# Optimization experiments

Hardware: AMD Instinct MI355X
Metric: run time of the kernel (lower is better)

Reference implementation:

```python
import jax, jax.numpy as jnp
import numpy as np

D_MODEL = 1024
HEAD = 16
EPS = 1e-6


def _norm(x, alpha, beta):
    # Faithful to NormalizeLayer: torch.std is unbiased (ddof=1); scalar alpha/bias.
    mean = jnp.mean(x, axis=-1, keepdims=True)
    std = jnp.std(x, axis=-1, ddof=1, keepdims=True)
    return alpha * ((x - mean) / (std + EPS)) + beta


def setup_inputs() -> dict:
    key = jax.random.key(0)
    ks = jax.random.split(key, 16)
    B, S, D = 4, 1024, D_MODEL
    s = 1.0 / np.sqrt(D)
    inp = {
        'x': jax.random.normal(ks[0], (B, S, D), dtype=jnp.float32),
        'mask': jnp.ones((B, 1, 1, S), dtype=jnp.int32),
        'Wq_w': jax.random.normal(ks[1], (D, D), dtype=jnp.float32) * s,
        'Wq_b': jnp.zeros((D,), dtype=jnp.float32),
        'Wk_w': jax.random.normal(ks[2], (D, D), dtype=jnp.float32) * s,
        'Wk_b': jnp.zeros((D,), dtype=jnp.float32),
        'Wv_w': jax.random.normal(ks[3], (D, D), dtype=jnp.float32) * s,
        'Wv_b': jnp.zeros((D,), dtype=jnp.float32),
        'Wo_w': jax.random.normal(ks[4], (D, D), dtype=jnp.float32) * s,
        'Wo_b': jnp.zeros((D,), dtype=jnp.float32),
        'ff1_w': jax.random.normal(ks[5], (D, D), dtype=jnp.float32) * s,
        'ff1_b': jnp.zeros((D,), dtype=jnp.float32),
        'ff2_w': jax.random.normal(ks[6], (D, D), dtype=jnp.float32) * s,
        'ff2_b': jnp.zeros((D,), dtype=jnp.float32),
        'alpha1': jnp.ones((1,), dtype=jnp.float32),
        'beta1': jnp.zeros((1,), dtype=jnp.float32),
        'alpha2': jnp.ones((1,), dtype=jnp.float32),
        'beta2': jnp.zeros((1,), dtype=jnp.float32),
    }
    return inp


def reference(x, mask, Wq_w, Wq_b, Wk_w, Wk_b, Wv_w, Wv_b, Wo_w, Wo_b,
              ff1_w, ff1_b, ff2_w, ff2_b, alpha1, beta1, alpha2, beta2):
    B, S, D = x.shape
    H = HEAD
    kd = D // H
    # QKV projections (torch Linear: y = x @ W.T + b)
    Q = (x @ Wq_w.T + Wq_b).reshape(B, S, H, kd).transpose(0, 2, 1, 3)
    K = (x @ Wk_w.T + Wk_b).reshape(B, S, H, kd).transpose(0, 2, 1, 3)
    V = (x @ Wv_w.T + Wv_b).reshape(B, S, H, kd).transpose(0, 2, 1, 3)
    score = jnp.einsum('bhqd,bhkd->bhqk', Q, K) / jnp.sqrt(jnp.float32(kd))
    score = jnp.where(mask == 0, -jnp.inf, score)
    attn = jax.nn.softmax(score, axis=-1)
    o = jnp.einsum('bhqk,bhkd->bhqd', attn, V)
    o = o.transpose(0, 2, 1, 3).reshape(B, S, D)
    attn_out = o @ Wo_w.T + Wo_b
    # residual 1 + custom norm (dropout is identity in eval / drop=0)
    x1 = _norm(x + attn_out, alpha1, beta1)
    # feed-forward: Linear -> ReLU -> Linear (both d_model x d_model)
    ff = jax.nn.relu(x1 @ ff1_w.T + ff1_b) @ ff2_w.T + ff2_b
    # residual 2 + custom norm
    return _norm(x1 + ff, alpha2, beta2)
```

## Files before the change

### kernel.cpp

```cpp
#include <hip/hip_runtime.h>


typedef __bf16 bf16x8 __attribute__((ext_vector_type(8)));
typedef float f32x4 __attribute__((ext_vector_type(4)));
typedef unsigned short ushort4v __attribute__((ext_vector_type(4)));

static __device__ __forceinline__ unsigned short f2bf(float f) {
  return __builtin_bit_cast(unsigned short, (__bf16)f);
}
static __device__ __forceinline__ float bf2f(unsigned short u) {
  return __builtin_bit_cast(float, (unsigned int)u << 16);
}

static __device__ __forceinline__ void gload_lds16(const void* g, void* l) {
  __builtin_amdgcn_global_load_lds(
      (const __attribute__((address_space(1))) unsigned int*)g,
      (__attribute__((address_space(3))) unsigned int*)l, 16, 0, 0);
}

__global__ __launch_bounds__(256)
void cvt_all(const float* __restrict__ x, const float* __restrict__ wq,
             const float* __restrict__ wk, const float* __restrict__ wv,
             const float* __restrict__ wo, const float* __restrict__ w1,
             const float* __restrict__ w2,
             unsigned short* __restrict__ x_bf, unsigned short* __restrict__ wqkv_bf,
             unsigned short* __restrict__ wo_bf, unsigned short* __restrict__ w1_bf,
             unsigned short* __restrict__ w2_bf) {
  const int y = blockIdx.y;
  const size_t MEL = 1u << 20;
  const float* src;
  unsigned short* dst;
  switch (y) {
    case 0: case 1: case 2: case 3: src = x + y * MEL; dst = x_bf + y * MEL; break;
    case 4: src = wq; dst = wqkv_bf; break;
    case 5: src = wk; dst = wqkv_bf + MEL; break;
    case 6: src = wv; dst = wqkv_bf + 2 * MEL; break;
    case 7: src = wo; dst = wo_bf; break;
    case 8: src = w1; dst = w1_bf; break;
    default: src = w2; dst = w2_bf; break;
  }
  const int i = blockIdx.x * 256 + threadIdx.x;
  const float4 v = reinterpret_cast<const float4*>(src)[i];
  ushort4v o;
  o[0] = f2bf(v.x); o[1] = f2bf(v.y); o[2] = f2bf(v.z); o[3] = f2bf(v.w);
  reinterpret_cast<ushort4v*>(dst)[i] = o;
}

template<bool RELU, int OUT_MODE>
__global__ __launch_bounds__(256, 2)
void gemm_bt(const unsigned short* __restrict__ A,
             const unsigned short* __restrict__ W,
             const float* __restrict__ bias0, const float* __restrict__ bias1,
             const float* __restrict__ bias2,
             void* __restrict__ out0, unsigned short* __restrict__ outK,
             unsigned short* __restrict__ outVt, int M, int N, int K) {
  __shared__ __align__(16) unsigned short Al[2][128][64];
  __shared__ __align__(16) unsigned short Bl[2][128][64];
  const int tid = threadIdx.x;
  const int lane = tid & 63;
  const int w = tid >> 6;
  const int wr = w >> 1, wc = w & 1;
  const int grp = lane >> 4, l15 = lane & 15;
  const long bRow = (long)blockIdx.x * 128;
  const long bCol = (long)blockIdx.y * 128;

  f32x4 acc[4][4];
#pragma unroll
  for (int m = 0; m < 4; m++)
#pragma unroll
    for (int n = 0; n < 4; n++) { f32x4 z = {0.f,0.f,0.f,0.f}; acc[m][n] = z; }

  const int srow = tid >> 3;
  const int xc = (((tid & 7) ^ (srow & 7)) << 3);
  const unsigned short* Ag[4];
  const unsigned short* Wg[4];
#pragma unroll
  for (int r = 0; r < 4; r++) {
    Ag[r] = A + (bRow + r * 32 + srow) * (long)K + xc;
    Wg[r] = W + (bCol + r * 32 + srow) * (long)K + xc;
  }

  auto stage = [&](int k0, int buf) {
    unsigned short* ldsA = &Al[buf][0][0] + w * 512;
    unsigned short* ldsB = &Bl[buf][0][0] + w * 512;
#pragma unroll
    for (int r = 0; r < 4; r++) {
      gload_lds16(Ag[r] + k0, ldsA + r * 2048);
      gload_lds16(Wg[r] + k0, ldsB + r * 2048);
    }
  };

  const int NT = K >> 6;
  stage(0, 0);
  for (int t = 0; t < NT; ++t) {
    const int cur = t & 1;
    __syncthreads();
    if (t + 1 < NT) stage((t + 1) << 6, cur ^ 1);
#pragma unroll
    for (int kk = 0; kk < 2; kk++) {
      bf16x8 af[4], bfr[4];
#pragma unroll
      for (int m = 0; m < 4; m++) {
        const int R = wr * 64 + m * 16 + l15;
        const int pos = (kk * 4 + grp) ^ (R & 7);
        af[m] = *(const bf16x8*)&Al[cur][R][pos << 3];
      }
#pragma unroll
      for (int n = 0; n < 4; n++) {
        const int R = wc * 64 + n * 16 + l15;
        const int pos = (kk * 4 + grp) ^ (R & 7);
        bfr[n] = *(const bf16x8*)&Bl[cur][R][pos << 3];
      }
#pragma unroll
      for (int m = 0; m < 4; m++)
#pragma unroll
        for (int n = 0; n < 4; n++)
          acc[m][n] = __builtin_amdgcn_mfma_f32_16x16x32_bf16(af[m], bfr[n], acc[m][n], 0, 0, 0);
    }
  }

  const float QSCL = 0.125f * 1.44269504088896340736f;
  const int seg = (OUT_MODE == 2) ? (int)(bCol >> 10) : 0;
  const float* bp = (OUT_MODE == 2) ? (seg == 0 ? bias0 : seg == 1 ? bias1 : bias2) : bias0;
#pragma unroll
  for (int n = 0; n < 4; n++) {
    const long col = bCol + wc * 64 + n * 16 + l15;
    const float bv = bp[OUT_MODE == 2 ? (col & 1023) : col];
#pragma unroll
    for (int m = 0; m < 4; m++) {
      const long row0 = bRow + wr * 64 + m * 16 + grp * 4;
#pragma unroll
      for (int r = 0; r < 4; r++) {
        float v = acc[m][n][r] + bv;
        if (RELU) v = fmaxf(v, 0.f);
        const long row = row0 + r;
        if (OUT_MODE == 1) {
          ((unsigned short*)out0)[row * (long)N + col] = f2bf(v);
        } else {
          if (seg == 0) {
            ((unsigned short*)out0)[row * 1024 + col] = f2bf(v * QSCL);
          } else if (seg == 1) {
            outK[row * 1024 + (col & 1023)] = f2bf(v);
          } else {
            const long vc = col & 1023;
            const long idx = (((row >> 10) * 16 + (vc >> 6)) << 16) + ((vc & 63) << 10) + (row & 1023);
            outVt[idx] = f2bf(v);
          }
        }
      }
    }
  }
}

__global__ __launch_bounds__(256)
void attn_kernel(const unsigned short* __restrict__ Qb,
                 const unsigned short* __restrict__ Kb,
                 const unsigned short* __restrict__ Vt_g,
                 const int* __restrict__ maskp,
                 unsigned short* __restrict__ Ob) {
  const int S = 1024, D = 1024;
  __shared__ __align__(16) unsigned short Kl[2][64][64];
  __shared__ __align__(16) unsigned short Vl[2][64][64];
  __shared__ __align__(16) unsigned short Pl[64][64];
  const int tid = threadIdx.x;
  const int lane = tid & 63;
  const int w = tid >> 6;
  const int grp = lane >> 4, l15 = lane & 15;
  const int bh = blockIdx.x;
  const int qt = blockIdx.y;
  const int b = bh >> 4, h = bh & 15;
  const float NEG = -__builtin_inff();

  const int4 mv = *(const int4*)(maskp + b * S + tid * 4);
  const int allLive = __syncthreads_and(mv.x && mv.y && mv.z && mv.w);

  const unsigned short* Qp = Qb + ((size_t)(b * S + qt * 64 + w * 16 + l15)) * D + h * 64;
  const bf16x8 aq0 = *(const bf16x8*)(Qp + grp * 8);
  const bf16x8 aq1 = *(const bf16x8*)(Qp + 32 + grp * 8);

  bf16x8 onesb;
#pragma unroll
  for (int j = 0; j < 8; j++) onesb[j] = (__bf16)1.0f;

  f32x4 acc_o[4];
#pragma unroll
  for (int f = 0; f < 4; f++) { f32x4 z = {0.f,0.f,0.f,0.f}; acc_o[f] = z; }
  f32x4 acc_l = {0.f, 0.f, 0.f, 0.f};
  float M = NEG;

  const int srow = tid >> 3;
  const int xc = (((tid & 7) ^ (srow & 7)) << 3);
  const unsigned short* Kg0 = Kb + ((size_t)(b * S + srow)) * D + h * 64 + xc;
  const unsigned short* Kg1 = Kg0 + 32 * (size_t)D;
  const unsigned short* Vgb = Vt_g + (((size_t)bh) << 16);
  const unsigned short* Vg0 = Vgb + (size_t)srow * S + xc;
  const unsigned short* Vg1 = Vg0 + 32 * (size_t)S;

  auto stage = [&](int kt2, int buf) {
    const size_t kb = (size_t)kt2 * 64;
    gload_lds16(Kg0 + kb * D, &Kl[buf][0][0] + w * 512);
    gload_lds16(Kg1 + kb * D, &Kl[buf][0][0] + w * 512 + 2048);
    gload_lds16(Vg0 + kb,     &Vl[buf][0][0] + w * 512);
    gload_lds16(Vg1 + kb,     &Vl[buf][0][0] + w * 512 + 2048);
  };
  stage(0, 0);

  for (int kt = 0; kt < 16; ++kt) {
    const int cur = kt & 1;
    const int kbase = kt * 64;
    __syncthreads();
    if (kt < 15) stage(kt + 1, cur ^ 1);

    f32x4 sfr[4];
    __builtin_amdgcn_s_setprio(1);
#pragma unroll
    for (int f = 0; f < 4; f++) {
      const int R = f * 16 + l15;
      const int p0 = (grp ^ (R & 7)) << 3;
      const int p1 = ((4 + grp) ^ (R & 7)) << 3;
      bf16x8 bk0 = *(const bf16x8*)&Kl[cur][R][p0];
      bf16x8 bk1 = *(const bf16x8*)&Kl[cur][R][p1];
      f32x4 z = {0.f,0.f,0.f,0.f};
      z = __builtin_amdgcn_mfma_f32_16x16x32_bf16(aq0, bk0, z, 0, 0, 0);
      z = __builtin_amdgcn_mfma_f32_16x16x32_bf16(aq1, bk1, z, 0, 0, 0);
      sfr[f] = z;
    }
    __builtin_amdgcn_s_setprio(0);

    if (!allLive) {
#pragma unroll
      for (int f = 0; f < 4; f++) {
        const float biasf = maskp[b * S + kbase + f * 16 + l15] ? 0.f : NEG;
#pragma unroll
        for (int r = 0; r < 4; r++) sfr[f][r] += biasf;
      }
    }

    float t0 = fmaxf(fmaxf(sfr[0][0], sfr[0][1]), sfr[0][2]);
    float t1 = fmaxf(fmaxf(sfr[0][3], sfr[1][0]), sfr[1][1]);
    float t2 = fmaxf(fmaxf(sfr[1][2], sfr[1][3]), sfr[2][0]);
    float t3 = fmaxf(fmaxf(sfr[2][1], sfr[2][2]), sfr[2][3]);
    float t4 = fmaxf(fmaxf(sfr[3][0], sfr[3][1]), sfr[3][2]);
    float rm = fmaxf(fmaxf(fmaxf(t0, t1), t2), fmaxf(fmaxf(t3, t4), sfr[3][3]));
    rm = fmaxf(rm, __shfl_xor(rm, 1));
    rm = fmaxf(rm, __shfl_xor(rm, 2));
    rm = fmaxf(rm, __shfl_xor(rm, 4));
    rm = fmaxf(rm, __shfl_xor(rm, 8));
    rm = fmaxf(rm, __shfl_xor(rm, 16));
    rm = fmaxf(rm, __shfl_xor(rm, 32));
    if (rm > M + 8.f) {
      const float sc = exp2f(M - rm);
      M = rm;
#pragma unroll
      for (int f = 0; f < 4; f++) acc_o[f] *= sc;
      acc_l *= sc;
    }

#pragma unroll
    for (int f = 0; f < 4; f++) {
#pragma unroll
      for (int r = 0; r < 4; r++) {
        const float p = exp2f(sfr[f][r] - M);
        const int q = w * 16 + grp * 4 + r;
        const int cchunk = (f * 2 + (l15 >> 3)) ^ (q & 7);
        ((unsigned short*)Pl)[q * 64 + (cchunk << 3) + (l15 & 7)] = f2bf(p);
      }
    }

    const int Rp = w * 16 + l15;
    const bf16x8 ap0 = *(const bf16x8*)&Pl[Rp][((grp ^ (Rp & 7)) << 3)];
    const bf16x8 ap1 = *(const bf16x8*)&Pl[Rp][(((4 + grp) ^ (Rp & 7)) << 3)];
    __builtin_amdgcn_s_setprio(1);
#pragma unroll
    for (int f = 0; f < 4; f++) {
      const int Rv = f * 16 + l15;
      bf16x8 bv0 = *(const bf16x8*)&Vl[cur][Rv][((grp ^ (Rv & 7)) << 3)];
      bf16x8 bv1 = *(const bf16x8*)&Vl[cur][Rv][(((4 + grp) ^ (Rv & 7)) << 3)];
      acc_o[f] = __builtin_amdgcn_mfma_f32_16x16x32_bf16(ap0, bv0, acc_o[f], 0, 0, 0);
      acc_o[f] = __builtin_amdgcn_mfma_f32_16x16x32_bf16(ap1, bv1, acc_o[f], 0, 0, 0);
    }
    acc_l = __builtin_amdgcn_mfma_f32_16x16x32_bf16(ap0, onesb, acc_l, 0, 0, 0);
    acc_l = __builtin_amdgcn_mfma_f32_16x16x32_bf16(ap1, onesb, acc_l, 0, 0, 0);
    __builtin_amdgcn_s_setprio(0);
  }

#pragma unroll
  for (int r = 0; r < 4; r++) {
    const float inv = 1.f / acc_l[r];
    const int row = qt * 64 + w * 16 + grp * 4 + r;
#pragma unroll
    for (int f = 0; f < 4; f++) {
      const float v = acc_o[f][r] * inv;
      Ob[((size_t)(b * S + row)) * D + h * 64 + f * 16 + l15] = f2bf(v);
    }
  }
}

template<int AMODE, int BMODE, bool F32OUT, bool BF16OUT>
__global__ __launch_bounds__(256)
void norm_residual(const void* __restrict__ a, const void* __restrict__ bsrc,
                   const float* __restrict__ alpha, const float* __restrict__ beta,
                   float* __restrict__ out, unsigned short* __restrict__ out_bf) {
  const int D = 1024;
  const size_t base = (size_t)blockIdx.x * D + threadIdx.x * 4;
  float a0, a1, a2, a3, b0v, b1v, b2v, b3v;
  if (AMODE == 0) {
    const float4 va = *(const float4*)((const float*)a + base);
    a0 = va.x; a1 = va.y; a2 = va.z; a3 = va.w;
  } else {
    const ushort4v va = *(const ushort4v*)((const unsigned short*)a + base);
    a0 = bf2f(va[0]); a1 = bf2f(va[1]); a2 = bf2f(va[2]); a3 = bf2f(va[3]);
  }
  if (BMODE == 0) {
    const float4 vb = *(const float4*)((const float*)bsrc + base);
    b0v = vb.x; b1v = vb.y; b2v = vb.z; b3v = vb.w;
  } else {
    const ushort4v vb = *(const ushort4v*)((const unsigned short*)bsrc + base);
    b0v = bf2f(vb[0]); b1v = bf2f(vb[1]); b2v = bf2f(vb[2]); b3v = bf2f(vb[3]);
  }
  const float x0 = a0 + b0v, x1 = a1 + b1v, x2 = a2 + b2v, x3 = a3 + b3v;
  float s1 = x0 + x1 + x2 + x3;
  float s2 = x0 * x0 + x1 * x1 + x2 * x2 + x3 * x3;
#pragma unroll
  for (int m = 1; m < 64; m <<= 1) {
    s1 += __shfl_xor(s1, m);
    s2 += __shfl_xor(s2, m);
  }
  __shared__ float red[8];
  const int w = threadIdx.x >> 6, lane = threadIdx.x & 63;
  if (lane == 0) { red[w] = s1; red[4 + w] = s2; }
  __syncthreads();
  s1 = red[0] + red[1] + red[2] + red[3];
  s2 = red[4] + red[5] + red[6] + red[7];
  const float mean = s1 * (1.f / 1024.f);
  const float var = fmaxf((s2 - 1024.f * mean * mean) * (1.f / 1023.f), 0.f);
  const float k = alpha[0] / (sqrtf(var) + 1e-6f);
  const float b0 = beta[0];
  const float y0 = (x0 - mean) * k + b0;
  const float y1 = (x1 - mean) * k + b0;
  const float y2 = (x2 - mean) * k + b0;
  const float y3 = (x3 - mean) * k + b0;
  if (F32OUT) {
    float4 o = {y0, y1, y2, y3};
    *(float4*)(out + base) = o;
  }
  if (BF16OUT) {
    ushort4v ob;
    ob[0] = f2bf(y0); ob[1] = f2bf(y1); ob[2] = f2bf(y2); ob[3] = f2bf(y3);
    *(ushort4v*)(out_bf + base) = ob;
  }
}

extern "C" void kernel_launch(void* const* d_in, const int* in_sizes, int n_in,
                              void* d_out, int out_size, void* d_ws, size_t ws_size,
                              hipStream_t stream) {
  const float* x      = (const float*)d_in[0];
  const int*   maskp  = (const int*)d_in[1];
  const float* Wq_w   = (const float*)d_in[2];
  const float* Wq_b   = (const float*)d_in[3];
  const float* Wk_w   = (const float*)d_in[4];
  const float* Wk_b   = (const float*)d_in[5];
  const float* Wv_w   = (const float*)d_in[6];
  const float* Wv_b   = (const float*)d_in[7];
  const float* Wo_w   = (const float*)d_in[8];
  const float* Wo_b   = (const float*)d_in[9];
  const float* W1_w   = (const float*)d_in[10];
  const float* W1_b   = (const float*)d_in[11];
  const float* W2_w   = (const float*)d_in[12];
  const float* W2_b   = (const float*)d_in[13];
  const float* alpha1 = (const float*)d_in[14];
  const float* beta1  = (const float*)d_in[15];
  const float* alpha2 = (const float*)d_in[16];
  const float* beta2  = (const float*)d_in[17];

  const int B = 4, S = 1024, D = 1024;
  const int M = B * S;
  const size_t MiB = 1u << 20;
  char* ws = (char*)d_ws;
  unsigned short* x_bf    = (unsigned short*)(ws + 0 * MiB);
  unsigned short* Wqkv_bf = (unsigned short*)(ws + 8 * MiB);
  unsigned short* Wo_bf   = (unsigned short*)(ws + 14 * MiB);
  unsigned short* W1_bf   = (unsigned short*)(ws + 16 * MiB);
  unsigned short* W2_bf   = (unsigned short*)(ws + 18 * MiB);
  unsigned short* Q_bf    = (unsigned short*)(ws + 20 * MiB);
  unsigned short* K_bf    = (unsigned short*)(ws + 28 * MiB);
  unsigned short* Vt_bf   = (unsigned short*)(ws + 36 * MiB);
  unsigned short* O_bf    = (unsigned short*)(ws + 44 * MiB);
  unsigned short* attn_bf = (unsigned short*)(ws + 52 * MiB);
  unsigned short* x1_bf   = (unsigned short*)(ws + 20 * MiB);
  unsigned short* ff1_bf  = (unsigned short*)(ws + 28 * MiB);
  unsigned short* ff2_bf  = (unsigned short*)(ws + 36 * MiB);

  cvt_all<<<dim3(1024, 10), dim3(256), 0, stream>>>(
      x, Wq_w, Wk_w, Wv_w, Wo_w, W1_w, W2_w, x_bf, Wqkv_bf, Wo_bf, W1_bf, W2_bf);

  gemm_bt<false, 2><<<dim3(M / 128, 24), dim3(256), 0, stream>>>(
      x_bf, Wqkv_bf, Wq_b, Wk_b, Wv_b, Q_bf, K_bf, Vt_bf, M, 3072, D);

  attn_kernel<<<dim3(B * 16, S / 64), dim3(256), 0, stream>>>(Q_bf, K_bf, Vt_bf, maskp, O_bf);

  gemm_bt<false, 1><<<dim3(M / 128, 8), dim3(256), 0, stream>>>(
      O_bf, Wo_bf, Wo_b, nullptr, nullptr, attn_bf, nullptr, nullptr, M, D, D);
  norm_residual<0, 1, false, true><<<dim3(M), dim3(256), 0, stream>>>(
      x, attn_bf, alpha1, beta1, nullptr, x1_bf);
  gemm_bt<true, 1><<<dim3(M / 128, 8), dim3(256), 0, stream>>>(
      x1_bf, W1_bf, W1_b, nullptr, nullptr, ff1_bf, nullptr, nullptr, M, D, D);
  gemm_bt<false, 1><<<dim3(M / 128, 8), dim3(256), 0, stream>>>(
      ff1_bf, W2_bf, W2_b, nullptr, nullptr, ff2_bf, nullptr, nullptr, M, D, D);
  norm_residual<1, 1, true, false><<<dim3(M), dim3(256), 0, stream>>>(
      x1_bf, ff2_bf, alpha2, beta2, (float*)d_out, nullptr);
}
```

Baseline: 186.9 us.

## Halve GEMM row tile and double attention query tile per block

The GEMM block tile shrinks from 128x128 to 64x128, doubling the grid so the 1024-wide projections spread over more compute units at the cost of less operand reuse per block. The attention kernel now processes 128 query rows per block (32 per wave), reusing each staged K/V tile across twice as many queries. This halves K/V global traffic but raises register pressure and LDS for the larger P buffer. The attention kernel also gets a launch-bounds occupancy hint.

```diff
diff --git a/kernel.cpp b/kernel.cpp
--- a/kernel.cpp
+++ b/kernel.cpp
@@ -54,40 +54,40 @@
              const float* __restrict__ bias2,
              void* __restrict__ out0, unsigned short* __restrict__ outK,
              unsigned short* __restrict__ outVt, int M, int N, int K) {
-  __shared__ __align__(16) unsigned short Al[2][128][64];
+  __shared__ __align__(16) unsigned short Al[2][64][64];
   __shared__ __align__(16) unsigned short Bl[2][128][64];
   const int tid = threadIdx.x;
   const int lane = tid & 63;
   const int w = tid >> 6;
   const int wr = w >> 1, wc = w & 1;
   const int grp = lane >> 4, l15 = lane & 15;
-  const long bRow = (long)blockIdx.x * 128;
+  const long bRow = (long)blockIdx.x * 64;
   const long bCol = (long)blockIdx.y * 128;
 
-  f32x4 acc[4][4];
-#pragma unroll
-  for (int m = 0; m < 4; m++)
+  f32x4 acc[2][4];
+#pragma unroll
+  for (int m = 0; m < 2; m++)
 #pragma unroll
     for (int n = 0; n < 4; n++) { f32x4 z = {0.f,0.f,0.f,0.f}; acc[m][n] = z; }
 
   const int srow = tid >> 3;
   const int xc = (((tid & 7) ^ (srow & 7)) << 3);
-  const unsigned short* Ag[4];
-  const unsigned short* Wg[4];
-#pragma unroll
-  for (int r = 0; r < 4; r++) {
-    Ag[r] = A + (bRow + r * 32 + srow) * (long)K + xc;
-    Wg[r] = W + (bCol + r * 32 + srow) * (long)K + xc;
-  }
+  const unsigned short* Ag0 = A + (bRow + srow) * (long)K + xc;
+  const unsigned short* Ag1 = Ag0 + 32L * K;
+  const unsigned short* Wg0 = W + (bCol + srow) * (long)K + xc;
+  const unsigned short* Wg1 = Wg0 + 32L * K;
+  const unsigned short* Wg2 = Wg0 + 64L * K;
+  const unsigned short* Wg3 = Wg0 + 96L * K;
 
   auto stage = [&](int k0, int buf) {
     unsigned short* ldsA = &Al[buf][0][0] + w * 512;
     unsigned short* ldsB = &Bl[buf][0][0] + w * 512;
-#pragma unroll
-    for (int r = 0; r < 4; r++) {
-      gload_lds16(Ag[r] + k0, ldsA + r * 2048);
-      gload_lds16(Wg[r] + k0, ldsB + r * 2048);
-    }
+    gload_lds16(Ag0 + k0, ldsA);
+    gload_lds16(Ag1 + k0, ldsA + 2048);
+    gload_lds16(Wg0 + k0, ldsB);
+    gload_lds16(Wg1 + k0, ldsB + 2048);
+    gload_lds16(Wg2 + k0, ldsB + 4096);
+    gload_lds16(Wg3 + k0, ldsB + 6144);
   };
 
   const int NT = K >> 6;
@@ -98,10 +98,10 @@
     if (t + 1 < NT) stage((t + 1) << 6, cur ^ 1);
 #pragma unroll
     for (int kk = 0; kk < 2; kk++) {
-      bf16x8 af[4], bfr[4];
-#pragma unroll
-      for (int m = 0; m < 4; m++) {
-        const int R = wr * 64 + m * 16 + l15;
+      bf16x8 af[2], bfr[4];
+#pragma unroll
+      for (int m = 0; m < 2; m++) {
+        const int R = wr * 32 + m * 16 + l15;
         const int pos = (kk * 4 + grp) ^ (R & 7);
         af[m] = *(const bf16x8*)&Al[cur][R][pos << 3];
       }
@@ -112,7 +112,7 @@
         bfr[n] = *(const bf16x8*)&Bl[cur][R][pos << 3];
       }
 #pragma unroll
-      for (int m = 0; m < 4; m++)
+      for (int m = 0; m < 2; m++)
 #pragma unroll
         for (int n = 0; n < 4; n++)
           acc[m][n] = __builtin_amdgcn_mfma_f32_16x16x32_bf16(af[m], bfr[n], acc[m][n], 0, 0, 0);
@@ -127,8 +127,8 @@
     const long col = bCol + wc * 64 + n * 16 + l15;
     const float bv = bp[OUT_MODE == 2 ? (col & 1023) : col];
 #pragma unroll
-    for (int m = 0; m < 4; m++) {
-      const long row0 = bRow + wr * 64 + m * 16 + grp * 4;
+    for (int m = 0; m < 2; m++) {
+      const long row0 = bRow + wr * 32 + m * 16 + grp * 4;
 #pragma unroll
       for (int r = 0; r < 4; r++) {
         float v = acc[m][n][r] + bv;
@@ -152,7 +152,7 @@
   }
 }
 
-__global__ __launch_bounds__(256)
+__global__ __launch_bounds__(256, 2)
 void attn_kernel(const unsigned short* __restrict__ Qb,
                  const unsigned short* __restrict__ Kb,
                  const unsigned short* __restrict__ Vt_g,
@@ -161,7 +161,7 @@
   const int S = 1024, D = 1024;
   __shared__ __align__(16) unsigned short Kl[2][64][64];
   __shared__ __align__(16) unsigned short Vl[2][64][64];
-  __shared__ __align__(16) unsigned short Pl[64][64];
+  __shared__ __align__(16) unsigned short Pl[128][64];
   const int tid = threadIdx.x;
   const int lane = tid & 63;
   const int w = tid >> 6;
@@ -174,18 +174,25 @@
   const int4 mv = *(const int4*)(maskp + b * S + tid * 4);
   const int allLive = __syncthreads_and(mv.x && mv.y && mv.z && mv.w);
 
-  const unsigned short* Qp = Qb + ((size_t)(b * S + qt * 64 + w * 16 + l15)) * D + h * 64;
-  const bf16x8 aq0 = *(const bf16x8*)(Qp + grp * 8);
-  const bf16x8 aq1 = *(const bf16x8*)(Qp + 32 + grp * 8);
+  bf16x8 aq[2][2];
+#pragma unroll
+  for (int m = 0; m < 2; m++) {
+    const unsigned short* Qp =
+        Qb + ((size_t)(b * S + qt * 128 + w * 32 + m * 16 + l15)) * D + h * 64;
+    aq[m][0] = *(const bf16x8*)(Qp + grp * 8);
+    aq[m][1] = *(const bf16x8*)(Qp + 32 + grp * 8);
+  }
 
   bf16x8 onesb;
 #pragma unroll
   for (int j = 0; j < 8; j++) onesb[j] = (__bf16)1.0f;
 
-  f32x4 acc_o[4];
-#pragma unroll
-  for (int f = 0; f < 4; f++) { f32x4 z = {0.f,0.f,0.f,0.f}; acc_o[f] = z; }
-  f32x4 acc_l = {0.f, 0.f, 0.f, 0.f};
+  f32x4 acc_o[2][4];
+#pragma unroll
+  for (int m = 0; m < 2; m++)
+#pragma unroll
+    for (int f = 0; f < 4; f++) { f32x4 z = {0.f,0.f,0.f,0.f}; acc_o[m][f] = z; }
+  f32x4 acc_l[2] = {{0.f,0.f,0.f,0.f}, {0.f,0.f,0.f,0.f}};
   float M = NEG;
 
   const int srow = tid >> 3;
@@ -211,7 +218,7 @@
     __syncthreads();
     if (kt < 15) stage(kt + 1, cur ^ 1);
 
-    f32x4 sfr[4];
+    f32x4 sfr[2][4];
     __builtin_amdgcn_s_setprio(1);
 #pragma unroll
     for (int f = 0; f < 4; f++) {
@@ -220,10 +227,13 @@
       const int p1 = ((4 + grp) ^ (R & 7)) << 3;
       bf16x8 bk0 = *(const bf16x8*)&Kl[cur][R][p0];
       bf16x8 bk1 = *(const bf16x8*)&Kl[cur][R][p1];
-      f32x4 z = {0.f,0.f,0.f,0.f};
-      z = __builtin_amdgcn_mfma_f32_16x16x32_bf16(aq0, bk0, z, 0, 0, 0);
-      z = __builtin_amdgcn_mfma_f32_16x16x32_bf16(aq1, bk1, z, 0, 0, 0);
-      sfr[f] = z;
+#pragma unroll
+      for (int m = 0; m < 2; m++) {
+        f32x4 z = {0.f,0.f,0.f,0.f};
+        z = __builtin_amdgcn_mfma_f32_16x16x32_bf16(aq[m][0], bk0, z, 0, 0, 0);
+        z = __builtin_amdgcn_mfma_f32_16x16x32_bf16(aq[m][1], bk1, z, 0, 0, 0);
+        sfr[m][f] = z;
+      }
     }
     __builtin_amdgcn_s_setprio(0);
 
@@ -232,16 +242,19 @@
       for (int f = 0; f < 4; f++) {
         const float biasf = maskp[b * S + kbase + f * 16 + l15] ? 0.f : NEG;
 #pragma unroll
-        for (int r = 0; r < 4; r++) sfr[f][r] += biasf;
-      }
-    }
-
-    float t0 = fmaxf(fmaxf(sfr[0][0], sfr[0][1]), sfr[0][2]);
-    float t1 = fmaxf(fmaxf(sfr[0][3], sfr[1][0]), sfr[1][1]);
-    float t2 = fmaxf(fmaxf(sfr[1][2], sfr[1][3]), sfr[2][0]);
-    float t3 = fmaxf(fmaxf(sfr[2][1], sfr[2][2]), sfr[2][3]);
-    float t4 = fmaxf(fmaxf(sfr[3][0], sfr[3][1]), sfr[3][2]);
-    float rm = fmaxf(fmaxf(fmaxf(t0, t1), t2), fmaxf(fmaxf(t3, t4), sfr[3][3]));
+        for (int m = 0; m < 2; m++)
+#pragma unroll
+          for (int r = 0; r < 4; r++) sfr[m][f][r] += biasf;
+      }
+    }
+
+    float rm = sfr[0][0][0];
+#pragma unroll
+    for (int m = 0; m < 2; m++)
+#pragma unroll
+      for (int f = 0; f < 4; f++)
+#pragma unroll
+        for (int r = 0; r < 4; r++) rm = fmaxf(rm, sfr[m][f][r]);
     rm = fmaxf(rm, __shfl_xor(rm, 1));
     rm = fmaxf(rm, __shfl_xor(rm, 2));
     rm = fmaxf(rm, __shfl_xor(rm, 4));
@@ -252,48 +265,62 @@
       const float sc = exp2f(M - rm);
       M = rm;
 #pragma unroll
-      for (int f = 0; f < 4; f++) acc_o[f] *= sc;
-      acc_l *= sc;
-    }
-
-#pragma unroll
-    for (int f = 0; f < 4; f++) {
-#pragma unroll
-      for (int r = 0; r < 4; r++) {
-        const float p = exp2f(sfr[f][r] - M);
-        const int q = w * 16 + grp * 4 + r;
-        const int cchunk = (f * 2 + (l15 >> 3)) ^ (q & 7);
-        ((unsigned short*)Pl)[q * 64 + (cchunk << 3) + (l15 & 7)] = f2bf(p);
-      }
-    }
-
-    const int Rp = w * 16 + l15;
-    const bf16x8 ap0 = *(const bf16x8*)&Pl[Rp][((grp ^ (Rp & 7)) << 3)];
-    const bf16x8 ap1 = *(const bf16x8*)&Pl[Rp][(((4 + grp) ^ (Rp & 7)) << 3)];
-    __builtin_amdgcn_s_setprio(1);
+      for (int m = 0; m < 2; m++) {
+#pragma unroll
+        for (int f = 0; f < 4; f++) acc_o[m][f] *= sc;
+        acc_l[m] *= sc;
+      }
+    }
+
+#pragma unroll
+    for (int m = 0; m < 2; m++)
+#pragma unroll
+      for (int f = 0; f < 4; f++)
+#pragma unroll
+        for (int r = 0; r < 4; r++) {
+          const float p = exp2f(sfr[m][f][r] - M);
+          const int q = w * 32 + m * 16 + grp * 4 + r;
+          const int cchunk = (f * 2 + (l15 >> 3)) ^ (q & 7);
+          ((unsigned short*)Pl)[q * 64 + (cchunk << 3) + (l15 & 7)] = f2bf(p);
+        }
+
+    bf16x8 bv0[4], bv1[4];
 #pragma unroll
     for (int f = 0; f < 4; f++) {
       const int Rv = f * 16 + l15;
-      bf16x8 bv0 = *(const bf16x8*)&Vl[cur][Rv][((grp ^ (Rv & 7)) << 3)];
-      bf16x8 bv1 = *(const bf16x8*)&Vl[cur][Rv][(((4 + grp) ^ (Rv & 7)) << 3)];
-      acc_o[f] = __builtin_amdgcn_mfma_f32_16x16x32_bf16(ap0, bv0, acc_o[f], 0, 0, 0);
-      acc_o[f] = __builtin_amdgcn_mfma_f32_16x16x32_bf16(ap1, bv1, acc_o[f], 0, 0, 0);
-    }
-    acc_l = __builtin_amdgcn_mfma_f32_16x16x32_bf16(ap0, onesb, acc_l, 0, 0, 0);
-    acc_l = __builtin_amdgcn_mfma_f32_16x16x32_bf16(ap1, onesb, acc_l, 0, 0, 0);
+      bv0[f] = *(const bf16x8*)&Vl[cur][Rv][((grp ^ (Rv & 7)) << 3)];
+      bv1[f] = *(const bf16x8*)&Vl[cur][Rv][(((4 + grp) ^ (Rv & 7)) << 3)];
+    }
+
+    __builtin_amdgcn_s_setprio(1);
+#pragma unroll
+    for (int m = 0; m < 2; m++) {
+      const int Rp = w * 32 + m * 16 + l15;
+      const bf16x8 ap0 = *(const bf16x8*)&Pl[Rp][((grp ^ (Rp & 7)) << 3)];
+      const bf16x8 ap1 = *(const bf16x8*)&Pl[Rp][(((4 + grp) ^ (Rp & 7)) << 3)];
+#pragma unroll
+      for (int f = 0; f < 4; f++) {
+        acc_o[m][f] = __builtin_amdgcn_mfma_f32_16x16x32_bf16(ap0, bv0[f], acc_o[m][f], 0, 0, 0);
+        acc_o[m][f] = __builtin_amdgcn_mfma_f32_16x16x32_bf16(ap1, bv1[f], acc_o[m][f], 0, 0, 0);
+      }
+      acc_l[m] = __builtin_amdgcn_mfma_f32_16x16x32_bf16(ap0, onesb, acc_l[m], 0, 0, 0);
+      acc_l[m] = __builtin_amdgcn_mfma_f32_16x16x32_bf16(ap1, onesb, acc_l[m], 0, 0, 0);
+    }
     __builtin_amdgcn_s_setprio(0);
   }
 
 #pragma unroll
-  for (int r = 0; r < 4; r++) {
-    const float inv = 1.f / acc_l[r];
-    const int row = qt * 64 + w * 16 + grp * 4 + r;
-#pragma unroll
-    for (int f = 0; f < 4; f++) {
-      const float v = acc_o[f][r] * inv;
-      Ob[((size_t)(b * S + row)) * D + h * 64 + f * 16 + l15] = f2bf(v);
-    }
-  }
+  for (int m = 0; m < 2; m++)
+#pragma unroll
+    for (int r = 0; r < 4; r++) {
+      const float inv = 1.f / acc_l[m][r];
+      const int row = qt * 128 + w * 32 + m * 16 + grp * 4 + r;
+#pragma unroll
+      for (int f = 0; f < 4; f++) {
+        const float v = acc_o[m][f][r] * inv;
+        Ob[((size_t)(b * S + row)) * D + h * 64 + f * 16 + l15] = f2bf(v);
+      }
+    }
 }
 
 template<int AMODE, int BMODE, bool F32OUT, bool BF16OUT>
@@ -394,18 +421,18 @@
   cvt_all<<<dim3(1024, 10), dim3(256), 0, stream>>>(
       x, Wq_w, Wk_w, Wv_w, Wo_w, W1_w, W2_w, x_bf, Wqkv_bf, Wo_bf, W1_bf, W2_bf);
 
-  gemm_bt<false, 2><<<dim3(M / 128, 24), dim3(256), 0, stream>>>(
+  gemm_bt<false, 2><<<dim3(M / 64, 24), dim3(256), 0, stream>>>(
       x_bf, Wqkv_bf, Wq_b, Wk_b, Wv_b, Q_bf, K_bf, Vt_bf, M, 3072, D);
 
-  attn_kernel<<<dim3(B * 16, S / 64), dim3(256), 0, stream>>>(Q_bf, K_bf, Vt_bf, maskp, O_bf);
-
-  gemm_bt<false, 1><<<dim3(M / 128, 8), dim3(256), 0, stream>>>(
+  attn_kernel<<<dim3(B * 16, S / 128), dim3(256), 0, stream>>>(Q_bf, K_bf, Vt_bf, maskp, O_bf);
+
+  gemm_bt<false, 1><<<dim3(M / 64, 8), dim3(256), 0, stream>>>(
       O_bf, Wo_bf, Wo_b, nullptr, nullptr, attn_bf, nullptr, nullptr, M, D, D);
   norm_residual<0, 1, false, true><<<dim3(M), dim3(256), 0, stream>>>(
       x, attn_bf, alpha1, beta1, nullptr, x1_bf);
-  gemm_bt<true, 1><<<dim3(M / 128, 8), dim3(256), 0, stream>>>(
+  gemm_bt<true, 1><<<dim3(M / 64, 8), dim3(256), 0, stream>>>(
       x1_bf, W1_bf, W1_b, nullptr, nullptr, ff1_bf, nullptr, nullptr, M, D, D);
-  gemm_bt<false, 1><<<dim3(M / 128, 8), dim3(256), 0, stream>>>(
+  gemm_bt<false, 1><<<dim3(M / 64, 8), dim3(256), 0, stream>>>(
       ff1_bf, W2_bf, W2_b, nullptr, nullptr, ff2_bf, nullptr, nullptr, M, D, D);
   norm_residual<1, 1, true, false><<<dim3(M), dim3(256), 0, stream>>>(
       x1_bf, ff2_bf, alpha2, beta2, (float*)d_out, nullptr);
```

Measured after the change: 158.3 us. 15.3% less time.
